# Optimization experiments

Hardware: AMD Instinct MI355X
Metric: run time of the kernel (lower is better)

Reference implementation:

```python
import jax, jax.numpy as jnp
import numpy as np
import math

HEAD = 4
HEAD_DIM = 16
K_ATT = 7
PAD_ATT = 3  # (dilation*(kernel_att-1)+1)//2 with dilation=1, kernel_att=7
K_CONV = 3


def closest_factor_to_sqrt(n):
    if n <= 1:
        return n
    sqrt_n = int(math.sqrt(n))
    if sqrt_n * sqrt_n == n:
        return sqrt_n
    best, best_diff = 1, float('inf')
    for i in range(sqrt_n, 0, -1):
        if n % i == 0:
            diff = abs(i - n // i)
            if diff < best_diff:
                best_diff, best = diff, i
    return best


def setup_inputs() -> dict:
    key = jax.random.key(0)
    ks = jax.random.split(key, 10)
    Cin, Cout = 64, 64
    x = jax.random.normal(ks[0], (2, Cin, 8, 32, 32), dtype=jnp.float32)
    w1 = jax.random.normal(ks[1], (Cout, Cin), dtype=jnp.float32) * 0.05
    b1 = jax.random.normal(ks[2], (Cout,), dtype=jnp.float32) * 0.01
    w2 = jax.random.normal(ks[3], (Cout, Cin), dtype=jnp.float32) * 0.05
    b2 = jax.random.normal(ks[4], (Cout,), dtype=jnp.float32) * 0.01
    w3 = jax.random.normal(ks[5], (Cout, Cin), dtype=jnp.float32) * 0.05
    b3 = jax.random.normal(ks[6], (Cout,), dtype=jnp.float32) * 0.01
    wp = jax.random.normal(ks[7], (HEAD_DIM, 3), dtype=jnp.float32) * 0.05
    bp = jnp.zeros((HEAD_DIM,), dtype=jnp.float32)
    wfc = jax.random.normal(ks[8], (K_CONV * K_CONV, 3 * HEAD), dtype=jnp.float32) * 0.05
    # dep_conv init per reset_parameters(): identity shift kernels, zero bias
    ident = jnp.eye(K_CONV * K_CONV, dtype=jnp.float32).reshape(K_CONV * K_CONV, K_CONV, K_CONV)
    wdep = jnp.tile(ident[None], (Cout, 1, 1, 1))  # (Cout, 9, 3, 3), groups=head_dim
    bdep = jnp.zeros((Cout,), dtype=jnp.float32)
    rate1 = jnp.array(0.5, dtype=jnp.float32)
    rate2 = jnp.array(0.5, dtype=jnp.float32)
    return {'x': x, 'w1': w1, 'b1': b1, 'w2': w2, 'b2': b2, 'w3': w3, 'b3': b3,
            'wp': wp, 'bp': bp, 'wfc': wfc, 'wdep': wdep, 'bdep': bdep,
            'rate1': rate1, 'rate2': rate2}


def _forward(x, w1, b1, w2, b2, w3, b3, wp, bp, wfc, wdep, bdep, rate1, rate2):
    conv1x1 = lambda t, wm, bias: jnp.einsum('oc,bcdwh->bodwh', wm, t) + bias[None, :, None, None, None]
    q = conv1x1(x, w1, b1)
    k = conv1x1(x, w2, b2)
    v = conv1x1(x, w3, b3)
    b, C, d, w, h = q.shape
    scaling = HEAD_DIM ** -0.5
    fh = closest_factor_to_sqrt(d)
    fw = d // fh
    H2, W2 = fh * h, fw * w  # flat reshape of (d, w, h) -> (H2, W2)

    # position encoding, torch position(d, h, w) -> (1, 3, d, w, h)
    loc_d = jnp.broadcast_to(jnp.linspace(-1.0, 1.0, d)[:, None, None], (d, w, h))
    loc_w = jnp.broadcast_to(jnp.linspace(-1.0, 1.0, w)[None, :, None], (d, w, h))
    loc_h = jnp.broadcast_to(jnp.linspace(-1.0, 1.0, h)[None, None, :], (d, w, h))
    loc = jnp.stack([loc_d, loc_w, loc_h], 0)[None].astype(x.dtype)
    pe = (jnp.einsum('oc,bcdwh->bodwh', wp, loc) + bp[None, :, None, None, None])
    pe = pe.reshape(1, HEAD_DIM, H2, W2)

    q_att = (q * scaling).reshape(b * HEAD, HEAD_DIM, H2, W2)
    k_att = k.reshape(b * HEAD, HEAD_DIM, H2, W2)
    v_att = v.reshape(b * HEAD, HEAD_DIM, H2, W2)

    def unfold(t):
        # nn.Unfold(kernel=7, stride=1) after ReflectionPad2d(3): (N, C, 49, H2, W2)
        p = jnp.pad(t, ((0, 0), (0, 0), (PAD_ATT, PAD_ATT), (PAD_ATT, PAD_ATT)), mode='reflect')
        return jnp.stack([p[:, :, i:i + H2, j:j + W2]
                          for i in range(K_ATT) for j in range(K_ATT)], axis=2)

    unfold_k = unfold(k_att)            # (b*head, hd, 49, H2, W2)
    unfold_rpe = unfold(pe)             # (1, hd, 49, H2, W2)
    scores = unfold_k + pe[:, :, None] - unfold_rpe
    att = jnp.einsum('nchw,nckhw->nkhw', q_att, scores)  # sum over head_dim
    att = jax.nn.softmax(att, axis=1)   # softmax over 49 window positions
    out_att = jnp.einsum('nkhw,nckhw->nchw', att, unfold(v_att))
    out_att = out_att.reshape(b, C, d, w, h)

    # conv-mixing branch
    L = d * w * h
    qkv = jnp.concatenate([q.reshape(b, HEAD, HEAD_DIM, L),
                           k.reshape(b, HEAD, HEAD_DIM, L),
                           v.reshape(b, HEAD, HEAD_DIM, L)], axis=1)  # (b, 3*head, hd, L)
    # fc: 1x1x1 conv over the 3*head channel axis (torch applies it unbatched after permute)
    f_all = jnp.einsum('oc,bcml->boml', wfc, qkv)         # (b, 9, hd, L)
    f_conv = f_all.reshape(b, K_CONV * K_CONV * HEAD_DIM, d, h * w)
    out_conv = jax.lax.conv_general_dilated(
        f_conv, wdep, window_strides=(1, 1), padding=[(1, 1), (1, 1)],
        dimension_numbers=('NCHW', 'OIHW', 'NCHW'), feature_group_count=HEAD_DIM)
    out_conv = out_conv + bdep[None, :, None, None]
    out_conv = out_conv.reshape(b, C, d, w, h)

    return rate1 * out_att + rate2 * out_conv


def reference(x, w1, b1, w2, b2, w3, b3, wp, bp, wfc, wdep, bdep, rate1, rate2):
    return _forward(x, w1, b1, w2, b2, w3, b3, wp, bp, wfc, wdep, bdep, rate1, rate2)
```

## Files before the change

kernel.cpp:

```cpp
#include <hip/hip_runtime.h>
#include <hip/hip_fp16.h>


static __device__ __forceinline__ float2 h2f2(float w) {
    __half2 h = *reinterpret_cast<__half2*>(&w);
    return __half22float2(h);
}

__global__ __launch_bounds__(512) void qkvf_kernel(
    const float* __restrict__ x,
    const float* __restrict__ w1, const float* __restrict__ b1,
    const float* __restrict__ w2, const float* __restrict__ b2,
    const float* __restrict__ w3, const float* __restrict__ b3,
    const float* __restrict__ wfc,
    float* __restrict__ q, float* __restrict__ k, float* __restrict__ v,
    float* __restrict__ f)
{
    __shared__ float xs[64][128];
    __shared__ float wlds[3][32][64];

    int bx    = blockIdx.x;
    int ltile = bx & 63;
    int half  = (bx >> 6) & 1;
    int b     = bx >> 7;
    int l0    = ltile * 128;
    int hdb   = half * 8;

    for (int t = threadIdx.x; t < 1536; t += 512) {
        int mat = t >> 9;
        int r   = t & 511;
        int cl  = r >> 4;
        int col = r & 15;
        int hh = cl >> 3, hdl = cl & 7;
        int c  = hh * 16 + hdb + hdl;
        const float* src = (mat == 0) ? w1 : (mat == 1) ? w2 : w3;
        ((float4*)wlds)[t] = ((const float4*)src)[c * 16 + col];
    }
    const float4* xg = (const float4*)(x + (size_t)b * 64 * 8192);
    for (int t = threadIdx.x; t < 2048; t += 512) {
        int ci = t >> 5, col = t & 31;
        ((float4*)xs)[t] = xg[ci * 2048 + (l0 >> 2) + col];
    }
    __syncthreads();

    int lane = threadIdx.x & 63;
    int wv   = __builtin_amdgcn_readfirstlane(threadIdx.x >> 6);
    int hd   = hdb + wv;
    int ll   = 2 * lane;

    float qa[4][2], ka[4][2], va[4][2];
#pragma unroll
    for (int hh = 0; hh < 4; ++hh) {
        int c = hh * 16 + hd;
        qa[hh][0] = qa[hh][1] = b1[c];
        ka[hh][0] = ka[hh][1] = b2[c];
        va[hh][0] = va[hh][1] = b3[c];
    }

#pragma unroll 4
    for (int c4 = 0; c4 < 16; ++c4) {
        float2 xv[4];
#pragma unroll
        for (int u = 0; u < 4; ++u)
            xv[u] = *(const float2*)&xs[c4 * 4 + u][ll];
#pragma unroll
        for (int hh = 0; hh < 4; ++hh) {
            int cl = hh * 8 + wv;
            float4 wq = *(const float4*)&wlds[0][cl][c4 * 4];
            float4 wk = *(const float4*)&wlds[1][cl][c4 * 4];
            float4 wx = *(const float4*)&wlds[2][cl][c4 * 4];
            qa[hh][0] = fmaf(wq.x, xv[0].x, qa[hh][0]);
            qa[hh][1] = fmaf(wq.x, xv[0].y, qa[hh][1]);
            qa[hh][0] = fmaf(wq.y, xv[1].x, qa[hh][0]);
            qa[hh][1] = fmaf(wq.y, xv[1].y, qa[hh][1]);
            qa[hh][0] = fmaf(wq.z, xv[2].x, qa[hh][0]);
            qa[hh][1] = fmaf(wq.z, xv[2].y, qa[hh][1]);
            qa[hh][0] = fmaf(wq.w, xv[3].x, qa[hh][0]);
            qa[hh][1] = fmaf(wq.w, xv[3].y, qa[hh][1]);

            ka[hh][0] = fmaf(wk.x, xv[0].x, ka[hh][0]);
            ka[hh][1] = fmaf(wk.x, xv[0].y, ka[hh][1]);
            ka[hh][0] = fmaf(wk.y, xv[1].x, ka[hh][0]);
            ka[hh][1] = fmaf(wk.y, xv[1].y, ka[hh][1]);
            ka[hh][0] = fmaf(wk.z, xv[2].x, ka[hh][0]);
            ka[hh][1] = fmaf(wk.z, xv[2].y, ka[hh][1]);
            ka[hh][0] = fmaf(wk.w, xv[3].x, ka[hh][0]);
            ka[hh][1] = fmaf(wk.w, xv[3].y, ka[hh][1]);

            va[hh][0] = fmaf(wx.x, xv[0].x, va[hh][0]);
            va[hh][1] = fmaf(wx.x, xv[0].y, va[hh][1]);
            va[hh][0] = fmaf(wx.y, xv[1].x, va[hh][0]);
            va[hh][1] = fmaf(wx.y, xv[1].y, va[hh][1]);
            va[hh][0] = fmaf(wx.z, xv[2].x, va[hh][0]);
            va[hh][1] = fmaf(wx.z, xv[2].y, va[hh][1]);
            va[hh][0] = fmaf(wx.w, xv[3].x, va[hh][0]);
            va[hh][1] = fmaf(wx.w, xv[3].y, va[hh][1]);
        }
    }

#pragma unroll
    for (int hh = 0; hh < 4; ++hh) {
        int c = hh * 16 + hd;
        size_t o = (size_t)(b * 64 + c) * 8192 + l0 + ll;
        *(float2*)&q[o] = make_float2(qa[hh][0] * 0.25f, qa[hh][1] * 0.25f);
        *(float2*)&k[o] = make_float2(ka[hh][0], ka[hh][1]);
        *(float2*)&v[o] = make_float2(va[hh][0], va[hh][1]);
    }

#pragma unroll
    for (int m = 0; m < 9; ++m) {
        float a0 = 0.f, a1 = 0.f;
#pragma unroll
        for (int hh = 0; hh < 4; ++hh) {
            a0 = fmaf(wfc[m * 12 + 0 + hh], qa[hh][0], a0);
            a1 = fmaf(wfc[m * 12 + 0 + hh], qa[hh][1], a1);
            a0 = fmaf(wfc[m * 12 + 4 + hh], ka[hh][0], a0);
            a1 = fmaf(wfc[m * 12 + 4 + hh], ka[hh][1], a1);
            a0 = fmaf(wfc[m * 12 + 8 + hh], va[hh][0], a0);
            a1 = fmaf(wfc[m * 12 + 8 + hh], va[hh][1], a1);
        }
        size_t o = ((size_t)(b * 9 + m) * 16 + hd) * 8192 + l0 + ll;
        *(float2*)&f[o] = make_float2(a0, a1);
    }
}

__global__ __launch_bounds__(512, 4) void att_kernel(
    const float* __restrict__ q, const float* __restrict__ k,
    const float* __restrict__ v,
    const float* __restrict__ wp, const float* __restrict__ bp,
    const float* __restrict__ rate1p, float* __restrict__ out)
{
    __shared__ float kpb[484 * 12];
    __shared__ float vtb[484 * 12];

    int bx = blockIdx.x;
    int xt = bx & 7;
    int yt = (bx >> 3) & 3;
    int n  = bx >> 5;
    int head = n & 3;
    int b    = n >> 2;
    int y0 = yt * 16, x0 = xt * 16;

    for (int e = threadIdx.x; e < 3872; e += 512) {
        int c2 = e & 7;
        int px = e >> 3;
        int ty = px / 22, tx = px % 22;
        int c0 = c2 * 2;
        int sy = y0 + ty - 3; if (sy < 0) sy = -sy; else if (sy >= 64)  sy = 126 - sy;
        int sx = x0 + tx - 3; if (sx < 0) sx = -sx; else if (sx >= 128) sx = 254 - sx;
        int l = sy * 128 + sx;
        size_t o = (size_t)(b * 64 + head * 16 + c0) * 8192 + l;
        float k0 = k[o], k1 = k[o + 8192];
        float v0 = v[o], v1 = v[o + 8192];
        int dd = l >> 10, r2 = l & 1023, ww = r2 >> 5, hh2 = r2 & 31;
        float ld = dd  * (2.0f / 7.0f)  - 1.0f;
        float lw = ww  * (2.0f / 31.0f) - 1.0f;
        float lh = hh2 * (2.0f / 31.0f) - 1.0f;
        float pe0 = bp[c0];
        pe0 = fmaf(wp[c0 * 3 + 0], ld, pe0);
        pe0 = fmaf(wp[c0 * 3 + 1], lw, pe0);
        pe0 = fmaf(wp[c0 * 3 + 2], lh, pe0);
        float pe1 = bp[c0 + 1];
        pe1 = fmaf(wp[c0 * 3 + 3], ld, pe1);
        pe1 = fmaf(wp[c0 * 3 + 4], lw, pe1);
        pe1 = fmaf(wp[c0 * 3 + 5], lh, pe1);
        __half2 hk = __floats2half2_rn(k0 - pe0, k1 - pe1);
        __half2 hv = __floats2half2_rn(v0, v1);
        kpb[px * 12 + c2] = *reinterpret_cast<float*>(&hk);
        vtb[px * 12 + c2] = *reinterpret_cast<float*>(&hv);
    }
    __syncthreads();

    int pix  = threadIdx.x >> 1;
    int part = threadIdx.x & 1;
    int tx = pix & 15, ty = pix >> 4;
    int l = (y0 + ty) * 128 + (x0 + tx);
    int cb = part * 8;

    float qc[8];
#pragma unroll
    for (int c = 0; c < 8; ++c)
        qc[c] = q[(size_t)(b * 64 + head * 16 + cb + c) * 8192 + l];

    float lg[49];
#pragma unroll
    for (int i = 0; i < 7; ++i)
#pragma unroll
        for (int j = 0; j < 7; ++j) {
            float4 r = *(const float4*)&kpb[((ty + i) * 22 + tx + j) * 12
                                            + part * 4];
            float2 u0 = h2f2(r.x), u1 = h2f2(r.y),
                   u2 = h2f2(r.z), u3 = h2f2(r.w);
            float acc =      qc[0] * u0.x;
            acc = fmaf(qc[1], u0.y, acc); acc = fmaf(qc[2], u1.x, acc);
            acc = fmaf(qc[3], u1.y, acc); acc = fmaf(qc[4], u2.x, acc);
            acc = fmaf(qc[5], u2.y, acc); acc = fmaf(qc[6], u3.x, acc);
            acc = fmaf(qc[7], u3.y, acc);
            lg[i * 7 + j] = acc;
        }
#pragma unroll
    for (int kk = 0; kk < 49; ++kk)
        lg[kk] += __shfl_xor(lg[kk], 1, 64);

    float mx = lg[0];
#pragma unroll
    for (int kk = 1; kk < 49; ++kk) mx = fmaxf(mx, lg[kk]);
    float se = 0.f;
#pragma unroll
    for (int kk = 0; kk < 49; ++kk) { lg[kk] = __expf(lg[kk] - mx); se += lg[kk]; }
    float scale = rate1p[0] / se;

    float oc[8];
#pragma unroll
    for (int c = 0; c < 8; ++c) oc[c] = 0.f;
#pragma unroll
    for (int i = 0; i < 7; ++i)
#pragma unroll
        for (int j = 0; j < 7; ++j) {
            float wgt = lg[i * 7 + j];
            float4 r = *(const float4*)&vtb[((ty + i) * 22 + tx + j) * 12
                                            + part * 4];
            float2 u0 = h2f2(r.x), u1 = h2f2(r.y),
                   u2 = h2f2(r.z), u3 = h2f2(r.w);
            oc[0] = fmaf(wgt, u0.x, oc[0]); oc[1] = fmaf(wgt, u0.y, oc[1]);
            oc[2] = fmaf(wgt, u1.x, oc[2]); oc[3] = fmaf(wgt, u1.y, oc[3]);
            oc[4] = fmaf(wgt, u2.x, oc[4]); oc[5] = fmaf(wgt, u2.y, oc[5]);
            oc[6] = fmaf(wgt, u3.x, oc[6]); oc[7] = fmaf(wgt, u3.y, oc[7]);
        }

#pragma unroll
    for (int c = 0; c < 8; ++c)
        out[(size_t)(b * 64 + head * 16 + cb + c) * 8192 + l] = oc[c] * scale;
}

__global__ __launch_bounds__(256) void conv_kernel(
    const float* __restrict__ f,
    const float* __restrict__ wdep, const float* __restrict__ bdep,
    const float* __restrict__ rate2p, float* __restrict__ out)
{
    __shared__ float ft[9][8][66];

    int bx = blockIdx.x;
    int xt = bx & 15;
    int g  = (bx >> 4) & 15;
    int b  = bx >> 8;
    int x0 = xt * 64;

    const int NE = 9 * 8 * 66;
    for (int e = threadIdx.x; e < NE; e += 256) {
        int xx  = e % 66;
        int rem = e / 66;
        int y = rem % 8, i = rem / 8;
        int gx = x0 + xx - 1;
        float val = 0.f;
        if (gx >= 0 && gx < 1024) {
            int c144 = g * 9 + i;
            val = f[((size_t)(b * 144 + c144)) * 8192 + y * 1024 + gx];
        }
        ft[i][y][xx] = val;
    }
    __syncthreads();

    int xl = threadIdx.x & 63;
    int op = __builtin_amdgcn_readfirstlane(threadIdx.x >> 6);
    int o  = g * 4 + op;
    float rate2 = rate2p[0];

    float acc[8];
#pragma unroll
    for (int y = 0; y < 8; ++y) acc[y] = 0.f;

    for (int i = 0; i < 9; ++i) {
        float fr[10][3];
#pragma unroll
        for (int dx = 0; dx < 3; ++dx) { fr[0][dx] = 0.f; fr[9][dx] = 0.f; }
#pragma unroll
        for (int y = 0; y < 8; ++y)
#pragma unroll
            for (int dx = 0; dx < 3; ++dx)
                fr[y + 1][dx] = ft[i][y][xl + dx];
#pragma unroll
        for (int ky = 0; ky < 3; ++ky)
#pragma unroll
            for (int kx = 0; kx < 3; ++kx) {
                float wvv = wdep[((o * 9 + i) * 3 + ky) * 3 + kx];
#pragma unroll
                for (int y = 0; y < 8; ++y)
                    acc[y] = fmaf(wvv, fr[y + ky][kx], acc[y]);
            }
    }

    float bd = bdep[o];
#pragma unroll
    for (int y = 0; y < 8; ++y) {
        size_t idx = (size_t)(b * 64 + o) * 8192 + y * 1024 + x0 + xl;
        out[idx] = out[idx] + rate2 * (acc[y] + bd);
    }
}

extern "C" void kernel_launch(void* const* d_in, const int* in_sizes, int n_in,
                              void* d_out, int out_size, void* d_ws, size_t ws_size,
                              hipStream_t stream)
{
    (void)in_sizes; (void)n_in; (void)out_size; (void)ws_size;
    const float* x     = (const float*)d_in[0];
    const float* w1    = (const float*)d_in[1];
    const float* b1    = (const float*)d_in[2];
    const float* w2    = (const float*)d_in[3];
    const float* b2    = (const float*)d_in[4];
    const float* w3    = (const float*)d_in[5];
    const float* b3    = (const float*)d_in[6];
    const float* wp    = (const float*)d_in[7];
    const float* bp    = (const float*)d_in[8];
    const float* wfc   = (const float*)d_in[9];
    const float* wdep  = (const float*)d_in[10];
    const float* bdep  = (const float*)d_in[11];
    const float* rate1 = (const float*)d_in[12];
    const float* rate2 = (const float*)d_in[13];
    float* out = (float*)d_out;

    float* wsf = (float*)d_ws;
    float* q = wsf;
    float* k = wsf + 1048576;
    float* v = wsf + 2097152;
    float* f = wsf + 3145728;

    qkvf_kernel<<<256, 512, 0, stream>>>(x, w1, b1, w2, b2, w3, b3, wfc,
                                         q, k, v, f);
    att_kernel <<<256, 512, 0, stream>>>(q, k, v, wp, bp, rate1, out);
    conv_kernel<<<512, 256, 0, stream>>>(f, wdep, bdep, rate2, out);
}
```

Baseline: 119.7 us.

## Store q/k/v/f intermediates as packed fp16 and fold positional encoding into producer

The projection kernel now writes q, k-minus-positional-encoding, v and the fc mixing output as packed half2 values in a channel-pair layout. This halves intermediate global traffic and removes the per-tile PE computation and conversion from the attention staging loop. Each thread computes two adjacent channels with a 256-thread block. The cost is fp16 rounding of q and f, which were previously fp32.

```diff
diff --git a/kernel.cpp b/kernel.cpp
--- a/kernel.cpp
+++ b/kernel.cpp
@@ -6,15 +6,20 @@
     __half2 h = *reinterpret_cast<__half2*>(&w);
     return __half22float2(h);
 }
-
-__global__ __launch_bounds__(512) void qkvf_kernel(
+static __device__ __forceinline__ float pack2(float a, float b) {
+    __half2 h = __floats2half2_rn(a, b);
+    return *reinterpret_cast<float*>(&h);
+}
+
+__global__ __launch_bounds__(256) void qkvf_kernel(
     const float* __restrict__ x,
     const float* __restrict__ w1, const float* __restrict__ b1,
     const float* __restrict__ w2, const float* __restrict__ b2,
     const float* __restrict__ w3, const float* __restrict__ b3,
     const float* __restrict__ wfc,
-    float* __restrict__ q, float* __restrict__ k, float* __restrict__ v,
-    float* __restrict__ f)
+    const float* __restrict__ wp, const float* __restrict__ bp,
+    float* __restrict__ q16, float* __restrict__ kp16,
+    float* __restrict__ v16, float* __restrict__ f16p)
 {
     __shared__ float xs[64][128];
     __shared__ float wlds[3][32][64];
@@ -26,7 +31,7 @@
     int l0    = ltile * 128;
     int hdb   = half * 8;
 
-    for (int t = threadIdx.x; t < 1536; t += 512) {
+    for (int t = threadIdx.x; t < 1536; t += 256) {
         int mat = t >> 9;
         int r   = t & 511;
         int cl  = r >> 4;
@@ -37,7 +42,7 @@
         ((float4*)wlds)[t] = ((const float4*)src)[c * 16 + col];
     }
     const float4* xg = (const float4*)(x + (size_t)b * 64 * 8192);
-    for (int t = threadIdx.x; t < 2048; t += 512) {
+    for (int t = threadIdx.x; t < 2048; t += 256) {
         int ci = t >> 5, col = t & 31;
         ((float4*)xs)[t] = xg[ci * 2048 + (l0 >> 2) + col];
     }
@@ -45,17 +50,18 @@
 
     int lane = threadIdx.x & 63;
     int wv   = __builtin_amdgcn_readfirstlane(threadIdx.x >> 6);
-    int hd   = hdb + wv;
     int ll   = 2 * lane;
 
-    float qa[4][2], ka[4][2], va[4][2];
-#pragma unroll
-    for (int hh = 0; hh < 4; ++hh) {
-        int c = hh * 16 + hd;
-        qa[hh][0] = qa[hh][1] = b1[c];
-        ka[hh][0] = ka[hh][1] = b2[c];
-        va[hh][0] = va[hh][1] = b3[c];
-    }
+    float qa[4][2][2], ka[4][2][2], va[4][2][2];
+#pragma unroll
+    for (int hh = 0; hh < 4; ++hh)
+#pragma unroll
+        for (int p = 0; p < 2; ++p) {
+            int c = hh * 16 + hdb + 2 * wv + p;
+            qa[hh][p][0] = qa[hh][p][1] = b1[c];
+            ka[hh][p][0] = ka[hh][p][1] = b2[c];
+            va[hh][p][0] = va[hh][p][1] = b3[c];
+        }
 
 #pragma unroll 4
     for (int c4 = 0; c4 < 16; ++c4) {
@@ -64,70 +70,109 @@
         for (int u = 0; u < 4; ++u)
             xv[u] = *(const float2*)&xs[c4 * 4 + u][ll];
 #pragma unroll
+        for (int hh = 0; hh < 4; ++hh)
+#pragma unroll
+            for (int p = 0; p < 2; ++p) {
+                int cl = hh * 8 + 2 * wv + p;
+                float4 wq = *(const float4*)&wlds[0][cl][c4 * 4];
+                float4 wk = *(const float4*)&wlds[1][cl][c4 * 4];
+                float4 wx = *(const float4*)&wlds[2][cl][c4 * 4];
+                qa[hh][p][0] = fmaf(wq.x, xv[0].x, qa[hh][p][0]);
+                qa[hh][p][1] = fmaf(wq.x, xv[0].y, qa[hh][p][1]);
+                qa[hh][p][0] = fmaf(wq.y, xv[1].x, qa[hh][p][0]);
+                qa[hh][p][1] = fmaf(wq.y, xv[1].y, qa[hh][p][1]);
+                qa[hh][p][0] = fmaf(wq.z, xv[2].x, qa[hh][p][0]);
+                qa[hh][p][1] = fmaf(wq.z, xv[2].y, qa[hh][p][1]);
+                qa[hh][p][0] = fmaf(wq.w, xv[3].x, qa[hh][p][0]);
+                qa[hh][p][1] = fmaf(wq.w, xv[3].y, qa[hh][p][1]);
+
+                ka[hh][p][0] = fmaf(wk.x, xv[0].x, ka[hh][p][0]);
+                ka[hh][p][1] = fmaf(wk.x, xv[0].y, ka[hh][p][1]);
+                ka[hh][p][0] = fmaf(wk.y, xv[1].x, ka[hh][p][0]);
+                ka[hh][p][1] = fmaf(wk.y, xv[1].y, ka[hh][p][1]);
+                ka[hh][p][0] = fmaf(wk.z, xv[2].x, ka[hh][p][0]);
+                ka[hh][p][1] = fmaf(wk.z, xv[2].y, ka[hh][p][1]);
+                ka[hh][p][0] = fmaf(wk.w, xv[3].x, ka[hh][p][0]);
+                ka[hh][p][1] = fmaf(wk.w, xv[3].y, ka[hh][p][1]);
+
+                va[hh][p][0] = fmaf(wx.x, xv[0].x, va[hh][p][0]);
+                va[hh][p][1] = fmaf(wx.x, xv[0].y, va[hh][p][1]);
+                va[hh][p][0] = fmaf(wx.y, xv[1].x, va[hh][p][0]);
+                va[hh][p][1] = fmaf(wx.y, xv[1].y, va[hh][p][1]);
+                va[hh][p][0] = fmaf(wx.z, xv[2].x, va[hh][p][0]);
+                va[hh][p][1] = fmaf(wx.z, xv[2].y, va[hh][p][1]);
+                va[hh][p][0] = fmaf(wx.w, xv[3].x, va[hh][p][0]);
+                va[hh][p][1] = fmaf(wx.w, xv[3].y, va[hh][p][1]);
+            }
+    }
+
+    int l  = l0 + ll;
+    int dd = l >> 10, r2c = l & 1023, ww2 = r2c >> 5, hh2 = r2c & 31;
+    float ld  = dd  * (2.0f / 7.0f)  - 1.0f;
+    float lw  = ww2 * (2.0f / 31.0f) - 1.0f;
+    float lh0 = hh2 * (2.0f / 31.0f) - 1.0f;
+    float lh1 = (hh2 + 1) * (2.0f / 31.0f) - 1.0f;
+
+#pragma unroll
+    for (int hh = 0; hh < 4; ++hh) {
+        int c0  = hh * 16 + hdb + 2 * wv;
+        int row = b * 32 + (c0 >> 1);
+        size_t o = (size_t)row * 8192 + l;
+
+        *(float2*)&q16[o] = make_float2(
+            pack2(qa[hh][0][0] * 0.25f, qa[hh][1][0] * 0.25f),
+            pack2(qa[hh][0][1] * 0.25f, qa[hh][1][1] * 0.25f));
+
+        float pe00 = bp[c0];
+        pe00 = fmaf(wp[c0 * 3 + 0], ld, pe00);
+        pe00 = fmaf(wp[c0 * 3 + 1], lw, pe00);
+        float pe01 = fmaf(wp[c0 * 3 + 2], lh1, pe00);
+        pe00 = fmaf(wp[c0 * 3 + 2], lh0, pe00);
+        float pe10 = bp[c0 + 1];
+        pe10 = fmaf(wp[c0 * 3 + 3], ld, pe10);
+        pe10 = fmaf(wp[c0 * 3 + 4], lw, pe10);
+        float pe11 = fmaf(wp[c0 * 3 + 5], lh1, pe10);
+        pe10 = fmaf(wp[c0 * 3 + 5], lh0, pe10);
+
+        *(float2*)&kp16[o] = make_float2(
+            pack2(ka[hh][0][0] - pe00, ka[hh][1][0] - pe10),
+            pack2(ka[hh][0][1] - pe01, ka[hh][1][1] - pe11));
+
+        *(float2*)&v16[o] = make_float2(
+            pack2(va[hh][0][0], va[hh][1][0]),
+            pack2(va[hh][0][1], va[hh][1][1]));
+    }
+
+#pragma unroll
+    for (int m = 0; m < 9; ++m) {
+        float f00 = 0.f, f01 = 0.f, f10 = 0.f, f11 = 0.f;
+#pragma unroll
         for (int hh = 0; hh < 4; ++hh) {
-            int cl = hh * 8 + wv;
-            float4 wq = *(const float4*)&wlds[0][cl][c4 * 4];
-            float4 wk = *(const float4*)&wlds[1][cl][c4 * 4];
-            float4 wx = *(const float4*)&wlds[2][cl][c4 * 4];
-            qa[hh][0] = fmaf(wq.x, xv[0].x, qa[hh][0]);
-            qa[hh][1] = fmaf(wq.x, xv[0].y, qa[hh][1]);
-            qa[hh][0] = fmaf(wq.y, xv[1].x, qa[hh][0]);
-            qa[hh][1] = fmaf(wq.y, xv[1].y, qa[hh][1]);
-            qa[hh][0] = fmaf(wq.z, xv[2].x, qa[hh][0]);
-            qa[hh][1] = fmaf(wq.z, xv[2].y, qa[hh][1]);
-            qa[hh][0] = fmaf(wq.w, xv[3].x, qa[hh][0]);
-            qa[hh][1] = fmaf(wq.w, xv[3].y, qa[hh][1]);
-
-            ka[hh][0] = fmaf(wk.x, xv[0].x, ka[hh][0]);
-            ka[hh][1] = fmaf(wk.x, xv[0].y, ka[hh][1]);
-            ka[hh][0] = fmaf(wk.y, xv[1].x, ka[hh][0]);
-            ka[hh][1] = fmaf(wk.y, xv[1].y, ka[hh][1]);
-            ka[hh][0] = fmaf(wk.z, xv[2].x, ka[hh][0]);
-            ka[hh][1] = fmaf(wk.z, xv[2].y, ka[hh][1]);
-            ka[hh][0] = fmaf(wk.w, xv[3].x, ka[hh][0]);
-            ka[hh][1] = fmaf(wk.w, xv[3].y, ka[hh][1]);
-
-            va[hh][0] = fmaf(wx.x, xv[0].x, va[hh][0]);
-            va[hh][1] = fmaf(wx.x, xv[0].y, va[hh][1]);
-            va[hh][0] = fmaf(wx.y, xv[1].x, va[hh][0]);
-            va[hh][1] = fmaf(wx.y, xv[1].y, va[hh][1]);
-            va[hh][0] = fmaf(wx.z, xv[2].x, va[hh][0]);
-            va[hh][1] = fmaf(wx.z, xv[2].y, va[hh][1]);
-            va[hh][0] = fmaf(wx.w, xv[3].x, va[hh][0]);
-            va[hh][1] = fmaf(wx.w, xv[3].y, va[hh][1]);
-        }
-    }
-
-#pragma unroll
-    for (int hh = 0; hh < 4; ++hh) {
-        int c = hh * 16 + hd;
-        size_t o = (size_t)(b * 64 + c) * 8192 + l0 + ll;
-        *(float2*)&q[o] = make_float2(qa[hh][0] * 0.25f, qa[hh][1] * 0.25f);
-        *(float2*)&k[o] = make_float2(ka[hh][0], ka[hh][1]);
-        *(float2*)&v[o] = make_float2(va[hh][0], va[hh][1]);
-    }
-
-#pragma unroll
-    for (int m = 0; m < 9; ++m) {
-        float a0 = 0.f, a1 = 0.f;
-#pragma unroll
-        for (int hh = 0; hh < 4; ++hh) {
-            a0 = fmaf(wfc[m * 12 + 0 + hh], qa[hh][0], a0);
-            a1 = fmaf(wfc[m * 12 + 0 + hh], qa[hh][1], a1);
-            a0 = fmaf(wfc[m * 12 + 4 + hh], ka[hh][0], a0);
-            a1 = fmaf(wfc[m * 12 + 4 + hh], ka[hh][1], a1);
-            a0 = fmaf(wfc[m * 12 + 8 + hh], va[hh][0], a0);
-            a1 = fmaf(wfc[m * 12 + 8 + hh], va[hh][1], a1);
-        }
-        size_t o = ((size_t)(b * 9 + m) * 16 + hd) * 8192 + l0 + ll;
-        *(float2*)&f[o] = make_float2(a0, a1);
+            float wq = wfc[m * 12 + 0 + hh];
+            float wk = wfc[m * 12 + 4 + hh];
+            float wx = wfc[m * 12 + 8 + hh];
+            f00 = fmaf(wq, qa[hh][0][0], f00);
+            f01 = fmaf(wq, qa[hh][0][1], f01);
+            f10 = fmaf(wq, qa[hh][1][0], f10);
+            f11 = fmaf(wq, qa[hh][1][1], f11);
+            f00 = fmaf(wk, ka[hh][0][0], f00);
+            f01 = fmaf(wk, ka[hh][0][1], f01);
+            f10 = fmaf(wk, ka[hh][1][0], f10);
+            f11 = fmaf(wk, ka[hh][1][1], f11);
+            f00 = fmaf(wx, va[hh][0][0], f00);
+            f01 = fmaf(wx, va[hh][0][1], f01);
+            f10 = fmaf(wx, va[hh][1][0], f10);
+            f11 = fmaf(wx, va[hh][1][1], f11);
+        }
+        int t = m * 8 + half * 4 + wv;
+        size_t o = (size_t)(b * 72 + t) * 8192 + l;
+        *(float2*)&f16p[o] = make_float2(pack2(f00, f10), pack2(f01, f11));
     }
 }
 
 __global__ __launch_bounds__(512, 4) void att_kernel(
-    const float* __restrict__ q, const float* __restrict__ k,
-    const float* __restrict__ v,
-    const float* __restrict__ wp, const float* __restrict__ bp,
+    const float* __restrict__ q16, const float* __restrict__ kp16,
+    const float* __restrict__ v16,
     const float* __restrict__ rate1p, float* __restrict__ out)
 {
     __shared__ float kpb[484 * 12];
@@ -145,29 +190,12 @@
         int c2 = e & 7;
         int px = e >> 3;
         int ty = px / 22, tx = px % 22;
-        int c0 = c2 * 2;
         int sy = y0 + ty - 3; if (sy < 0) sy = -sy; else if (sy >= 64)  sy = 126 - sy;
         int sx = x0 + tx - 3; if (sx < 0) sx = -sx; else if (sx >= 128) sx = 254 - sx;
         int l = sy * 128 + sx;
-        size_t o = (size_t)(b * 64 + head * 16 + c0) * 8192 + l;
-        float k0 = k[o], k1 = k[o + 8192];
-        float v0 = v[o], v1 = v[o + 8192];
-        int dd = l >> 10, r2 = l & 1023, ww = r2 >> 5, hh2 = r2 & 31;
-        float ld = dd  * (2.0f / 7.0f)  - 1.0f;
-        float lw = ww  * (2.0f / 31.0f) - 1.0f;
-        float lh = hh2 * (2.0f / 31.0f) - 1.0f;
-        float pe0 = bp[c0];
-        pe0 = fmaf(wp[c0 * 3 + 0], ld, pe0);
-        pe0 = fmaf(wp[c0 * 3 + 1], lw, pe0);
-        pe0 = fmaf(wp[c0 * 3 + 2], lh, pe0);
-        float pe1 = bp[c0 + 1];
-        pe1 = fmaf(wp[c0 * 3 + 3], ld, pe1);
-        pe1 = fmaf(wp[c0 * 3 + 4], lw, pe1);
-        pe1 = fmaf(wp[c0 * 3 + 5], lh, pe1);
-        __half2 hk = __floats2half2_rn(k0 - pe0, k1 - pe1);
-        __half2 hv = __floats2half2_rn(v0, v1);
-        kpb[px * 12 + c2] = *reinterpret_cast<float*>(&hk);
-        vtb[px * 12 + c2] = *reinterpret_cast<float*>(&hv);
+        size_t o = (size_t)(b * 32 + head * 8 + c2) * 8192 + l;
+        kpb[px * 12 + c2] = kp16[o];
+        vtb[px * 12 + c2] = v16[o];
     }
     __syncthreads();
 
@@ -179,8 +207,11 @@
 
     float qc[8];
 #pragma unroll
-    for (int c = 0; c < 8; ++c)
-        qc[c] = q[(size_t)(b * 64 + head * 16 + cb + c) * 8192 + l];
+    for (int j = 0; j < 4; ++j) {
+        float w = q16[(size_t)(b * 32 + head * 8 + part * 4 + j) * 8192 + l];
+        float2 u = h2f2(w);
+        qc[2 * j] = u.x; qc[2 * j + 1] = u.y;
+    }
 
     float lg[49];
 #pragma unroll
@@ -234,7 +265,7 @@
 }
 
 __global__ __launch_bounds__(256) void conv_kernel(
-    const float* __restrict__ f,
+    const float* __restrict__ f16p,
     const float* __restrict__ wdep, const float* __restrict__ bdep,
     const float* __restrict__ rate2p, float* __restrict__ out)
 {
@@ -255,7 +286,10 @@
         float val = 0.f;
         if (gx >= 0 && gx < 1024) {
             int c144 = g * 9 + i;
-            val = f[((size_t)(b * 144 + c144)) * 8192 + y * 1024 + gx];
+            float wd = f16p[(size_t)(b * 72 + (c144 >> 1)) * 8192
+                            + y * 1024 + gx];
+            float2 u = h2f2(wd);
+            val = (c144 & 1) ? u.y : u.x;
         }
         ft[i][y][xx] = val;
     }
@@ -319,14 +353,14 @@
     const float* rate2 = (const float*)d_in[13];
     float* out = (float*)d_out;
 
-    float* wsf = (float*)d_ws;
-    float* q = wsf;
-    float* k = wsf + 1048576;
-    float* v = wsf + 2097152;
-    float* f = wsf + 3145728;
-
-    qkvf_kernel<<<256, 512, 0, stream>>>(x, w1, b1, w2, b2, w3, b3, wfc,
-                                         q, k, v, f);
-    att_kernel <<<256, 512, 0, stream>>>(q, k, v, wp, bp, rate1, out);
-    conv_kernel<<<512, 256, 0, stream>>>(f, wdep, bdep, rate2, out);
-}
+    float* wsf  = (float*)d_ws;
+    float* q16  = wsf;
+    float* kp16 = wsf + 524288;
+    float* v16  = wsf + 1048576;
+    float* f16p = wsf + 1572864;
+
+    qkvf_kernel<<<256, 256, 0, stream>>>(x, w1, b1, w2, b2, w3, b3, wfc,
+                                         wp, bp, q16, kp16, v16, f16p);
+    att_kernel <<<256, 512, 0, stream>>>(q16, kp16, v16, rate1, out);
+    conv_kernel<<<512, 256, 0, stream>>>(f16p, wdep, bdep, rate2, out);
+}
```

Result: slower. 126.9 us (+6.0%).
